# Kernel optimization log

Hardware: AMD Instinct MI355X
Metric: run time of the kernel (lower is better)

## Reference

```python
import jax, jax.numpy as jnp
import numpy as np

B = 1048576
IN_DIM, M, N = 3, 3, 16
C = 2            # num_per_level
W = 1000         # level_dim
MAX_FREQ = 10.0
A_CUBIC = -0.75  # torch grid_sample bicubic coefficient


def setup_inputs() -> dict:
    key = jax.random.key(0)
    k1, k2, k3, k4 = jax.random.split(key, 4)
    x = jax.random.normal(k1, (B, IN_DIM), dtype=jnp.float32)
    # stacked ParameterList of grids: each (1, C, 1, W) -> [N, C, W]
    grids = 0.1 * jax.random.normal(k2, (N, C, W), dtype=jnp.float32)
    G = jax.random.normal(k3, (IN_DIM, M, N), dtype=jnp.float32) * MAX_FREQ
    H = jax.random.normal(k4, (M, N), dtype=jnp.float32) * MAX_FREQ
    return {"x": x, "grids": grids, "G": G, "H": H, "size": 1}


def _cubic_inner(s):
    # weight for |s| <= 1
    return ((A_CUBIC + 2.0) * s - (A_CUBIC + 3.0)) * s * s + 1.0


def _cubic_outer(s):
    # weight for 1 < |s| < 2
    return ((A_CUBIC * s - 5.0 * A_CUBIC) * s + 8.0 * A_CUBIC) * s - 4.0 * A_CUBIC


def reference(x, grids, G, H, size):
    b = x.shape[0]
    in_dim, m, n = G.shape
    w = grids.shape[-1]
    # sin-feature projection: gx[b, i] in [-1, 1]
    a = (x @ G.reshape(in_dim, m * n)).reshape(b, m, n)
    gx = jnp.prod(jnp.sin(a + H.reshape(1, m, n)), axis=1)  # [B, N]
    # grid_sample, mode='bicubic', align_corners=False, padding_mode='zeros'.
    # y coordinate is 0 on an H=1 grid -> ty = 0 -> y-weights are [0,1,0,0],
    # so the 2D bicubic reduces exactly to 1D cubic along W with zero padding.
    ix = ((gx + 1.0) * w - 1.0) / 2.0  # unnormalize (align_corners=False)
    x0 = jnp.floor(ix)
    t = ix - x0
    base = x0.astype(jnp.int32)
    wts = (_cubic_outer(t + 1.0), _cubic_inner(t), _cubic_inner(1.0 - t), _cubic_outer(2.0 - t))
    lvl = jnp.arange(n)[None, :]  # [1, N] -> broadcasts against [B, N] indices
    out = jnp.zeros((b, n, grids.shape[1]), dtype=x.dtype)
    for k in range(4):  # 4 cubic taps (fixed small loop)
        idx = base + (k - 1)
        valid = (idx >= 0) & (idx < w)  # zeros padding for OOB taps
        idxc = jnp.clip(idx, 0, w - 1)
        vals = grids[lvl, :, idxc]  # [B, N, C] gather
        out = out + vals * (wts[k] * valid)[..., None]
    # per-level emb is [B, C]; concat over levels -> [B, N*C]
    return out.reshape(b, -1)
```

## Files before the change

kernel.cpp:

```cpp
#include <hip/hip_runtime.h>
#include <hip/hip_fp16.h>


constexpr int B_TOT = 1048576;
constexpr float A_C = -0.75f;

#define BLK 1024
#define WPAD 1004

__device__ __forceinline__ float hw_sin(float a) {
    float rev = a * 0.15915494309189535f;
    rev = __builtin_amdgcn_fractf(rev);
    return __builtin_amdgcn_sinf(rev);
}

__global__ __launch_bounds__(BLK, 8)
void trig_hashgrid(const float* __restrict__ x, const float* __restrict__ grids,
                   const float* __restrict__ G, const float* __restrict__ H,
                   float* __restrict__ out)
{
    __shared__ __half2 lds[8 * WPAD];
    const int tid  = threadIdx.x;
    const int half = blockIdx.x & 1;
    const int blk  = blockIdx.x >> 1;

    if (tid < 32) {
        int nl = tid >> 2, j = tid & 3;
        int off = (j < 2) ? j : (WPAD - 4 + j);
        lds[nl * WPAD + off] = __floats2half2_rn(0.0f, 0.0f);
    }
    {
        int row = tid >> 7;
        int j   = tid & 127;
        const float* gsrc = grids + half * 16000 + row * 2000;
        __half2* ldst = lds + row * WPAD;
        for (int w = j; w < 1000; w += 128)
            ldst[w + 2] = __floats2half2_rn(gsrc[w], gsrc[1000 + w]);
    }

    const int n_loc = tid & 7;
    const int n     = half * 8 + n_loc;
    const int g     = tid >> 3;

    float G0[3], G1[3], G2[3], Hr[3];
#pragma unroll
    for (int m = 0; m < 3; ++m) {
        G0[m] = G[0 * 48 + m * 16 + n];
        G1[m] = G[1 * 48 + m * 16 + n];
        G2[m] = G[2 * 48 + m * 16 + n];
        Hr[m] = H[m * 16 + n];
    }
    __syncthreads();

    float2* __restrict__ out2 = (float2*)out;
    const __half2* lrow = &lds[n_loc * WPAD];

    int b = blk * 128 + g;
    float x0 = x[b * 3 + 0];
    float x1 = x[b * 3 + 1];
    float x2 = x[b * 3 + 2];

#pragma unroll 2
    for (int i = 0; i < 16; ++i) {
        const int bn = b + 512 * 128;
        const int bs = (i < 15) ? bn : b;
        float y0 = x[bs * 3 + 0];
        float y1 = x[bs * 3 + 1];
        float y2 = x[bs * 3 + 2];

        float p = 1.0f;
#pragma unroll
        for (int m = 0; m < 3; ++m) {
            float a = fmaf(x0, G0[m], fmaf(x1, G1[m], fmaf(x2, G2[m], Hr[m])));
            p *= hw_sin(a);
        }

        float ix = fmaf(p, 500.0f, 499.5f);
        float xf = floorf(ix);
        float t  = ix - xf;
        int base = (int)xf;
        base = min(max(base, -1), 999);

        float u   = 1.0f - t;
        float tu  = t * u;
        float atu = A_C * tu;
        float w0  = atu * u;
        float w3  = atu * t;
        float w1  = fmaf(fmaf(A_C + 2.0f, t, -(A_C + 3.0f)), t * t, 1.0f);
        float w2  = 1.0f - w0 - w1 - w3;

        const __half2* tap = lrow + (base + 1);
        float2 v0 = __half22float2(tap[0]);
        float2 v1 = __half22float2(tap[1]);
        float2 v2 = __half22float2(tap[2]);
        float2 v3 = __half22float2(tap[3]);

        float o0 = v0.x * w0, o1 = v0.y * w0;
        o0 = fmaf(v1.x, w1, o0); o1 = fmaf(v1.y, w1, o1);
        o0 = fmaf(v2.x, w2, o0); o1 = fmaf(v2.y, w2, o1);
        o0 = fmaf(v3.x, w3, o0); o1 = fmaf(v3.y, w3, o1);

        out2[b * 16 + n] = make_float2(o0, o1);

        b = bn; x0 = y0; x1 = y1; x2 = y2;
    }
}

extern "C" void kernel_launch(void* const* d_in, const int* in_sizes, int n_in,
                              void* d_out, int out_size, void* d_ws, size_t ws_size,
                              hipStream_t stream) {
    const float* x     = (const float*)d_in[0];
    const float* grids = (const float*)d_in[1];
    const float* G     = (const float*)d_in[2];
    const float* H     = (const float*)d_in[3];
    float* out = (float*)d_out;
    trig_hashgrid<<<1024, BLK, 0, stream>>>(x, grids, G, H, out);
}
```

Measured before the change: 183.9 us.

## Software-pipeline LDS tap loads and blend taps with packed half2 FMA

Restructures the per-thread loop into a two-stage software pipeline: the next sample's sin projection, weights and LDS tap reads are issued before the current sample's blend and store, so LDS latency overlaps with compute. The 4-tap blend now runs in packed half2 multiply/FMA instead of converting each tap to float, cutting ALU instructions. The half-precision accumulation reduces output accuracy and holds more registers live across iterations.

```diff
diff --git a/kernel.cpp b/kernel.cpp
--- a/kernel.cpp
+++ b/kernel.cpp
@@ -2,7 +2,6 @@
 #include <hip/hip_fp16.h>
 
 
-constexpr int B_TOT = 1048576;
 constexpr float A_C = -0.75f;
 
 #define BLK 1024
@@ -12,6 +11,40 @@
     float rev = a * 0.15915494309189535f;
     rev = __builtin_amdgcn_fractf(rev);
     return __builtin_amdgcn_sinf(rev);
+}
+
+__device__ __forceinline__ void make_stage(
+    float x0, float x1, float x2,
+    const float G0[3], const float G1[3], const float G2[3], const float Hr[3],
+    const __half2* lrow,
+    __half2& W0, __half2& W1, __half2& W2, __half2& W3,
+    const __half2*& tap)
+{
+    float p = 1.0f;
+#pragma unroll
+    for (int m = 0; m < 3; ++m) {
+        float a = fmaf(x0, G0[m], fmaf(x1, G1[m], fmaf(x2, G2[m], Hr[m])));
+        p *= hw_sin(a);
+    }
+    float ix = fmaf(p, 500.0f, 499.5f);
+    float xf = floorf(ix);
+    float t  = ix - xf;
+    int base = (int)xf;
+    base = min(max(base, -1), 999);
+
+    float u   = 1.0f - t;
+    float tu  = t * u;
+    float atu = A_C * tu;
+    float w0  = atu * u;
+    float w3  = atu * t;
+    float w1  = fmaf(fmaf(A_C + 2.0f, t, -(A_C + 3.0f)), t * t, 1.0f);
+    float w2  = 1.0f - w0 - w1 - w3;
+
+    W0 = __float2half2_rn(w0);
+    W1 = __float2half2_rn(w1);
+    W2 = __float2half2_rn(w2);
+    W3 = __float2half2_rn(w3);
+    tap = lrow + (base + 1);
 }
 
 __global__ __launch_bounds__(BLK, 8)
@@ -55,54 +88,45 @@
     float2* __restrict__ out2 = (float2*)out;
     const __half2* lrow = &lds[n_loc * WPAD];
 
-    int b = blk * 128 + g;
-    float x0 = x[b * 3 + 0];
-    float x1 = x[b * 3 + 1];
-    float x2 = x[b * 3 + 2];
+    int b  = blk * 128 + g;
+    int b1 = b + 65536;
 
-#pragma unroll 2
-    for (int i = 0; i < 16; ++i) {
-        const int bn = b + 512 * 128;
-        const int bs = (i < 15) ? bn : b;
-        float y0 = x[bs * 3 + 0];
-        float y1 = x[bs * 3 + 1];
-        float y2 = x[bs * 3 + 2];
+    float y0, y1, y2;
+    __half2 W0, W1, W2, W3, t0, t1, t2, t3;
+    const __half2* tp;
 
-        float p = 1.0f;
-#pragma unroll
-        for (int m = 0; m < 3; ++m) {
-            float a = fmaf(x0, G0[m], fmaf(x1, G1[m], fmaf(x2, G2[m], Hr[m])));
-            p *= hw_sin(a);
-        }
+    {
+        float x0 = x[b * 3 + 0], x1 = x[b * 3 + 1], x2 = x[b * 3 + 2];
+        make_stage(x0, x1, x2, G0, G1, G2, Hr, lrow, W0, W1, W2, W3, tp);
+        t0 = tp[0]; t1 = tp[1]; t2 = tp[2]; t3 = tp[3];
+        y0 = x[b1 * 3 + 0]; y1 = x[b1 * 3 + 1]; y2 = x[b1 * 3 + 2];
+    }
 
-        float ix = fmaf(p, 500.0f, 499.5f);
-        float xf = floorf(ix);
-        float t  = ix - xf;
-        int base = (int)xf;
-        base = min(max(base, -1), 999);
+#pragma unroll 3
+    for (int i = 0; i < 15; ++i) {
+        __half2 nW0, nW1, nW2, nW3;
+        const __half2* ntp;
+        make_stage(y0, y1, y2, G0, G1, G2, Hr, lrow, nW0, nW1, nW2, nW3, ntp);
+        __half2 u0 = ntp[0], u1 = ntp[1], u2 = ntp[2], u3 = ntp[3];
+        int b2 = (i < 14) ? b1 + 65536 : b1;
+        float z0 = x[b2 * 3 + 0], z1 = x[b2 * 3 + 1], z2 = x[b2 * 3 + 2];
+        __half2 acc = __hmul2(t0, W0);
+        acc = __hfma2(t1, W1, acc);
+        acc = __hfma2(t2, W2, acc);
+        acc = __hfma2(t3, W3, acc);
+        out2[b * 16 + n] = __half22float2(acc);
+        b = b1; b1 = b2;
+        y0 = z0; y1 = z1; y2 = z2;
+        W0 = nW0; W1 = nW1; W2 = nW2; W3 = nW3;
+        t0 = u0;  t1 = u1;  t2 = u2;  t3 = u3;
+    }
 
-        float u   = 1.0f - t;
-        float tu  = t * u;
-        float atu = A_C * tu;
-        float w0  = atu * u;
-        float w3  = atu * t;
-        float w1  = fmaf(fmaf(A_C + 2.0f, t, -(A_C + 3.0f)), t * t, 1.0f);
-        float w2  = 1.0f - w0 - w1 - w3;
-
-        const __half2* tap = lrow + (base + 1);
-        float2 v0 = __half22float2(tap[0]);
-        float2 v1 = __half22float2(tap[1]);
-        float2 v2 = __half22float2(tap[2]);
-        float2 v3 = __half22float2(tap[3]);
-
-        float o0 = v0.x * w0, o1 = v0.y * w0;
-        o0 = fmaf(v1.x, w1, o0); o1 = fmaf(v1.y, w1, o1);
-        o0 = fmaf(v2.x, w2, o0); o1 = fmaf(v2.y, w2, o1);
-        o0 = fmaf(v3.x, w3, o0); o1 = fmaf(v3.y, w3, o1);
-
-        out2[b * 16 + n] = make_float2(o0, o1);
-
-        b = bn; x0 = y0; x1 = y1; x2 = y2;
+    {
+        __half2 acc = __hmul2(t0, W0);
+        acc = __hfma2(t1, W1, acc);
+        acc = __hfma2(t2, W2, acc);
+        acc = __hfma2(t3, W3, acc);
+        out2[b * 16 + n] = __half22float2(acc);
     }
 }
 
```

New measurement: 187.4 us. About the same (+1.9%).

## Process two levels per thread with 16-byte nontemporal stores and half2 FMAs

Applied to the files above, without the earlier changes.

Each thread now handles two adjacent levels and writes a 16-byte vector with a nontemporal store, instead of two 8-byte stores split across two block halves. Each block stages all 16 levels in LDS, so the grid shrinks to 512 blocks. The cubic interpolation now runs with packed half2 FMAs rather than fp32, which lowers arithmetic precision. The x prefetch software pipelining is dropped, and doubling the LDS footprint may reduce occupancy.

```diff
diff --git a/kernel.cpp b/kernel.cpp
--- a/kernel.cpp
+++ b/kernel.cpp
@@ -2,11 +2,12 @@
 #include <hip/hip_fp16.h>
 
 
-constexpr int B_TOT = 1048576;
 constexpr float A_C = -0.75f;
 
 #define BLK 1024
 #define WPAD 1004
+
+typedef float f32x4 __attribute__((ext_vector_type(4)));
 
 __device__ __forceinline__ float hw_sin(float a) {
     float rev = a * 0.15915494309189535f;
@@ -19,90 +20,84 @@
                    const float* __restrict__ G, const float* __restrict__ H,
                    float* __restrict__ out)
 {
-    __shared__ __half2 lds[8 * WPAD];
-    const int tid  = threadIdx.x;
-    const int half = blockIdx.x & 1;
-    const int blk  = blockIdx.x >> 1;
+    __shared__ __half2 lds[16 * WPAD];
+    const int tid = threadIdx.x;
+    const int blk = blockIdx.x;
 
-    if (tid < 32) {
+    if (tid < 64) {
         int nl = tid >> 2, j = tid & 3;
         int off = (j < 2) ? j : (WPAD - 4 + j);
         lds[nl * WPAD + off] = __floats2half2_rn(0.0f, 0.0f);
     }
     {
-        int row = tid >> 7;
-        int j   = tid & 127;
-        const float* gsrc = grids + half * 16000 + row * 2000;
+        int row = tid >> 6;
+        int j   = tid & 63;
+        const float* gsrc = grids + row * 2000;
         __half2* ldst = lds + row * WPAD;
-        for (int w = j; w < 1000; w += 128)
+        for (int w = j; w < 1000; w += 64)
             ldst[w + 2] = __floats2half2_rn(gsrc[w], gsrc[1000 + w]);
     }
 
-    const int n_loc = tid & 7;
-    const int n     = half * 8 + n_loc;
-    const int g     = tid >> 3;
+    const int np = tid & 7;
+    const int g  = tid >> 3;
+    const int n0 = 2 * np, n1 = n0 + 1;
 
-    float G0[3], G1[3], G2[3], Hr[3];
+    float Ga[2][3], Gb[2][3], Gc[2][3], Hh[2][3];
 #pragma unroll
     for (int m = 0; m < 3; ++m) {
-        G0[m] = G[0 * 48 + m * 16 + n];
-        G1[m] = G[1 * 48 + m * 16 + n];
-        G2[m] = G[2 * 48 + m * 16 + n];
-        Hr[m] = H[m * 16 + n];
+        Ga[0][m] = G[0*48 + m*16 + n0]; Ga[1][m] = G[0*48 + m*16 + n1];
+        Gb[0][m] = G[1*48 + m*16 + n0]; Gb[1][m] = G[1*48 + m*16 + n1];
+        Gc[0][m] = G[2*48 + m*16 + n0]; Gc[1][m] = G[2*48 + m*16 + n1];
+        Hh[0][m] = H[m*16 + n0];        Hh[1][m] = H[m*16 + n1];
     }
     __syncthreads();
 
-    float2* __restrict__ out2 = (float2*)out;
-    const __half2* lrow = &lds[n_loc * WPAD];
-
-    int b = blk * 128 + g;
-    float x0 = x[b * 3 + 0];
-    float x1 = x[b * 3 + 1];
-    float x2 = x[b * 3 + 2];
+    f32x4* __restrict__ out4 = (f32x4*)out;
+    const __half2* lrow0 = &lds[n0 * WPAD];
+    const __half2* lrow1 = &lds[n1 * WPAD];
 
 #pragma unroll 2
     for (int i = 0; i < 16; ++i) {
-        const int bn = b + 512 * 128;
-        const int bs = (i < 15) ? bn : b;
-        float y0 = x[bs * 3 + 0];
-        float y1 = x[bs * 3 + 1];
-        float y2 = x[bs * 3 + 2];
+        int b = blk * 128 + g + i * 65536;
+        float x0 = x[b * 3 + 0];
+        float x1 = x[b * 3 + 1];
+        float x2 = x[b * 3 + 2];
 
-        float p = 1.0f;
+        float2 o[2];
 #pragma unroll
-        for (int m = 0; m < 3; ++m) {
-            float a = fmaf(x0, G0[m], fmaf(x1, G1[m], fmaf(x2, G2[m], Hr[m])));
-            p *= hw_sin(a);
+        for (int s = 0; s < 2; ++s) {
+            float p = 1.0f;
+#pragma unroll
+            for (int m = 0; m < 3; ++m) {
+                float a = fmaf(x0, Ga[s][m],
+                          fmaf(x1, Gb[s][m],
+                          fmaf(x2, Gc[s][m], Hh[s][m])));
+                p *= hw_sin(a);
+            }
+            float ix = fmaf(p, 500.0f, 499.5f);
+            float xf = floorf(ix);
+            float t  = ix - xf;
+            int base = (int)xf;
+            base = min(max(base, -1), 999);
+
+            float u   = 1.0f - t;
+            float tu  = t * u;
+            float atu = A_C * tu;
+            float w0  = atu * u;
+            float w3  = atu * t;
+            float w1  = fmaf(fmaf(A_C + 2.0f, t, -(A_C + 3.0f)), t * t, 1.0f);
+            float w2  = 1.0f - w0 - w1 - w3;
+
+            const __half2* tap = (s ? lrow1 : lrow0) + (base + 1);
+            __half2 acc = __hmul2(tap[0], __float2half2_rn(w0));
+            acc = __hfma2(tap[1], __float2half2_rn(w1), acc);
+            acc = __hfma2(tap[2], __float2half2_rn(w2), acc);
+            acc = __hfma2(tap[3], __float2half2_rn(w3), acc);
+            o[s] = __half22float2(acc);
         }
 
-        float ix = fmaf(p, 500.0f, 499.5f);
-        float xf = floorf(ix);
-        float t  = ix - xf;
-        int base = (int)xf;
-        base = min(max(base, -1), 999);
-
-        float u   = 1.0f - t;
-        float tu  = t * u;
-        float atu = A_C * tu;
-        float w0  = atu * u;
-        float w3  = atu * t;
-        float w1  = fmaf(fmaf(A_C + 2.0f, t, -(A_C + 3.0f)), t * t, 1.0f);
-        float w2  = 1.0f - w0 - w1 - w3;
-
-        const __half2* tap = lrow + (base + 1);
-        float2 v0 = __half22float2(tap[0]);
-        float2 v1 = __half22float2(tap[1]);
-        float2 v2 = __half22float2(tap[2]);
-        float2 v3 = __half22float2(tap[3]);
-
-        float o0 = v0.x * w0, o1 = v0.y * w0;
-        o0 = fmaf(v1.x, w1, o0); o1 = fmaf(v1.y, w1, o1);
-        o0 = fmaf(v2.x, w2, o0); o1 = fmaf(v2.y, w2, o1);
-        o0 = fmaf(v3.x, w3, o0); o1 = fmaf(v3.y, w3, o1);
-
-        out2[b * 16 + n] = make_float2(o0, o1);
-
-        b = bn; x0 = y0; x1 = y1; x2 = y2;
+        f32x4 v = { o[0].x, o[0].y, o[1].x, o[1].y };
+        __builtin_nontemporal_store(v, &out4[b * 8 + np]);
     }
 }
 
@@ -114,5 +109,5 @@
     const float* G     = (const float*)d_in[2];
     const float* H     = (const float*)d_in[3];
     float* out = (float*)d_out;
-    trig_hashgrid<<<1024, BLK, 0, stream>>>(x, grids, G, H, out);
+    trig_hashgrid<<<512, BLK, 0, stream>>>(x, grids, G, H, out);
 }
```

Measured after the change: 173.1 us. 1.06x faster.
